# Optimization experiments

Hardware: AMD Instinct MI355X
Metric: run time of the kernel (lower is better)

## Reference

```python
import jax, jax.numpy as jnp
import numpy as np

# ---- static config ----
B, H, W, C = 32, 64, 64, 256
WS, SHIFT, NH = 8, 4, 8
HD = C // NH
N = WS * WS  # tokens per window
NW = (H // WS) * (W // WS)
EPS = 1e-5


def _relative_position_index(ws):
    ch, cw = np.meshgrid(np.arange(ws), np.arange(ws), indexing='ij')
    coords = np.stack([ch, cw]).reshape(2, -1)          # (2, N)
    rel = coords[:, :, None] - coords[:, None, :]        # (2, N, N)
    rel = rel.transpose(1, 2, 0)
    rel[:, :, 0] += ws - 1
    rel[:, :, 1] += ws - 1
    rel[:, :, 0] *= 2 * ws - 1
    return jnp.asarray(rel.sum(-1))                      # (N, N) int


def _shifted_window_mask(h, w, ws, shift):
    img = np.zeros((h, w))
    slices = (slice(0, -ws), slice(-ws, -shift), slice(-shift, None))
    cnt = 0
    for hs in slices:
        for wsl in slices:
            img[hs, wsl] = cnt
            cnt += 1
    mw = img.reshape(h // ws, ws, w // ws, ws).transpose(0, 2, 1, 3).reshape(-1, ws * ws)
    diff = mw[:, None, :] - mw[:, :, None]
    return jnp.asarray(np.where(diff != 0, -100.0, 0.0).astype(np.float32))  # (nW, N, N)


REL_IDX = _relative_position_index(WS)
ATTN_MASK = _shifted_window_mask(H, W, WS, SHIFT)


def _layernorm(x, g, b):
    mu = jnp.mean(x, axis=-1, keepdims=True)
    var = jnp.mean(jnp.square(x - mu), axis=-1, keepdims=True)
    return (x - mu) * jax.lax.rsqrt(var + EPS) * g + b


def _window_partition(x):  # (B,H,W,C) -> (B*nW, N, C)
    x = x.reshape(B, H // WS, WS, W // WS, WS, C)
    return x.transpose(0, 1, 3, 2, 4, 5).reshape(-1, N, C)


def _window_reverse(win):  # (B*nW, N, C) -> (B,H,W,C)
    x = win.reshape(B, H // WS, W // WS, WS, WS, C)
    return x.transpose(0, 1, 3, 2, 4, 5).reshape(B, H, W, C)


def setup_inputs() -> dict:
    key = jax.random.key(0)
    ks = jax.random.split(key, 6)
    s = lambda fan_in: 1.0 / np.sqrt(fan_in)
    return {
        'x': jax.random.normal(ks[0], (B, H * W, C), jnp.float32),
        'norm1_g': jnp.ones((C,), jnp.float32),
        'norm1_b': jnp.zeros((C,), jnp.float32),
        'qkv_w': jax.random.normal(ks[1], (C, 3 * C), jnp.float32) * s(C),
        'qkv_b': jnp.zeros((3 * C,), jnp.float32),
        'proj_w': jax.random.normal(ks[2], (C, C), jnp.float32) * s(C),
        'proj_b': jnp.zeros((C,), jnp.float32),
        'bias_table': jax.random.normal(ks[3], ((2 * WS - 1) ** 2, NH), jnp.float32) * 0.02,
        'norm2_g': jnp.ones((C,), jnp.float32),
        'norm2_b': jnp.zeros((C,), jnp.float32),
        'fc1_w': jax.random.normal(ks[4], (C, 4 * C), jnp.float32) * s(C),
        'fc1_b': jnp.zeros((4 * C,), jnp.float32),
        'fc2_w': jax.random.normal(ks[5], (4 * C, C), jnp.float32) * s(4 * C),
        'fc2_b': jnp.zeros((C,), jnp.float32),
    }


def reference(x, norm1_g, norm1_b, qkv_w, qkv_b, proj_w, proj_b, bias_table,
              norm2_g, norm2_b, fc1_w, fc1_b, fc2_w, fc2_b):
    shortcut = x
    h = _layernorm(x, norm1_g, norm1_b).reshape(B, H, W, C)
    # cyclic shift
    h = jnp.roll(h, shift=(-SHIFT, -SHIFT), axis=(1, 2))
    xw = _window_partition(h)                               # (Bw, N, C), Bw = B*nW
    # window attention
    qkv = xw @ qkv_w + qkv_b                                 # (Bw, N, 3C)
    qkv = qkv.reshape(-1, N, 3, NH, HD).transpose(2, 0, 3, 1, 4)
    q, k, v = qkv[0], qkv[1], qkv[2]                         # (Bw, NH, N, HD)
    attn = jnp.einsum('whnd,whmd->whnm', q * (HD ** -0.5), k)
    rpb = bias_table[REL_IDX.reshape(-1)].reshape(N, N, NH).transpose(2, 0, 1)
    attn = attn + rpb[None]
    attn = attn.reshape(B, NW, NH, N, N) + ATTN_MASK[None, :, None]
    attn = jax.nn.softmax(attn.reshape(-1, NH, N, N), axis=-1)
    out = jnp.einsum('whnm,whmd->whnd', attn, v)
    out = out.transpose(0, 2, 1, 3).reshape(-1, N, C)
    out = out @ proj_w + proj_b
    # reverse windows + shift back
    h = _window_reverse(out)
    h = jnp.roll(h, shift=(SHIFT, SHIFT), axis=(1, 2)).reshape(B, H * W, C)
    x = shortcut + h
    # MLP with pre-norm residual
    m = _layernorm(x, norm2_g, norm2_b)
    m = jax.nn.gelu(m @ fc1_w + fc1_b, approximate=False) @ fc2_w + fc2_b
    return x + m
```

## Files before the change

kernel.cpp:

```cpp
#include <hip/hip_runtime.h>
#include <hip/hip_bf16.h>


typedef __bf16 bf16;
typedef __bf16 bf16x8 __attribute__((ext_vector_type(8)));
typedef __bf16 bf16x4 __attribute__((ext_vector_type(4)));
typedef float  f32x4  __attribute__((ext_vector_type(4)));

#define GLDS(gp, lp)                                                                   \
    __builtin_amdgcn_global_load_lds(                                                  \
        (const __attribute__((address_space(1))) unsigned int*)(gp),                   \
        (__attribute__((address_space(3))) unsigned int*)(lp), 16, 0, 0)

__global__ __launch_bounds__(256) void prep_all(const float* __restrict__ qkv_w,
                                                const float* __restrict__ proj_w,
                                                const float* __restrict__ fc1_w,
                                                const float* __restrict__ fc2_w,
                                                const float* __restrict__ bt,
                                                bf16* __restrict__ WQ, bf16* __restrict__ WP,
                                                bf16* __restrict__ W1, bf16* __restrict__ W2,
                                                float* __restrict__ rpb) {
    int idx = blockIdx.x * 256 + threadIdx.x;
    if (idx < 196608) {
        int k = idx / 768, n = idx - k * 768;
        WQ[(size_t)n * 256 + k] = (bf16)qkv_w[idx];
    } else if (idx < 262144) {
        int l = idx - 196608;
        int k = l >> 8, n = l & 255;
        WP[(size_t)n * 256 + k] = (bf16)proj_w[l];
    } else if (idx < 524288) {
        int l = idx - 262144;
        int k = l >> 10, n = l & 1023;
        W1[(size_t)n * 256 + k] = (bf16)fc1_w[l];
    } else if (idx < 786432) {
        int l = idx - 524288;
        int k = l >> 8, n = l & 255;
        W2[(size_t)n * 1024 + k] = (bf16)fc2_w[l];
    } else {
        int l = idx - 786432;
        int h = l >> 12, n = (l >> 6) & 63, m = l & 63;
        int ridx = ((n >> 3) - (m >> 3) + 7) * 15 + ((n & 7) - (m & 7) + 7);
        rpb[l] = bt[ridx * 8 + h];
    }
}

__global__ __launch_bounds__(256) void ln_k(const float* __restrict__ x,
                                            const float* __restrict__ g,
                                            const float* __restrict__ bb,
                                            bf16* __restrict__ dst) {
    int t = blockIdx.x * 4 + (threadIdx.x >> 6);
    int lane = threadIdx.x & 63;
    int w = t >> 6, n = t & 63;
    int b = w >> 6, nw = w & 63;
    int r = ((nw >> 3) * 8 + (n >> 3) + 4) & 63;
    int c = ((nw & 7) * 8 + (n & 7) + 4) & 63;
    size_t src = ((size_t)b * 4096 + r * 64 + c) * 256;
    float4 v = *(const float4*)&x[src + lane * 4];
    float s = v.x + v.y + v.z + v.w;
    float sq = v.x * v.x + v.y * v.y + v.z * v.z + v.w * v.w;
#pragma unroll
    for (int off = 1; off < 64; off <<= 1) {
        s += __shfl_xor(s, off);
        sq += __shfl_xor(sq, off);
    }
    float mean = s * (1.0f / 256.0f);
    float var = sq * (1.0f / 256.0f) - mean * mean;
    float rstd = rsqrtf(var + 1e-5f);
    float4 gg = *(const float4*)&g[lane * 4];
    float4 bv = *(const float4*)&bb[lane * 4];
    bf16x4 o;
    o[0] = (bf16)((v.x - mean) * rstd * gg.x + bv.x);
    o[1] = (bf16)((v.y - mean) * rstd * gg.y + bv.y);
    o[2] = (bf16)((v.z - mean) * rstd * gg.z + bv.z);
    o[3] = (bf16)((v.w - mean) * rstd * gg.w + bv.w);
    *(bf16x4*)&dst[(size_t)t * 256 + lane * 4] = o;
}

__device__ __forceinline__ float fast_gelu(float v) {
    float t = v * v;
    float w = __builtin_fmaf(0.044715f * t, v, v);
    float e = __expf(-1.5957691216057308f * w);
    return v * __builtin_amdgcn_rcpf(1.0f + e);
}

template <int NDIM, int KDIM, int EPI>
__global__ __launch_bounds__(256) void gemm_k(const bf16* __restrict__ A,
                                              const bf16* __restrict__ Bt,
                                              const float* __restrict__ bias,
                                              bf16* __restrict__ outb,
                                              float* __restrict__ outf,
                                              const bf16* __restrict__ baseb) {
    __shared__ __align__(16) bf16 SH[24576];
    constexpr int NBN = NDIM / 128;
    constexpr int NK = KDIM / 32;
    const int tid = threadIdx.x;
    const int nwg = gridDim.x;
    const int flat = blockIdx.x;
    const int cpx = nwg >> 3;
    const int orig = (flat & 7) * cpx + (flat >> 3);
    const int bm = orig / NBN, bn = orig % NBN;

    const int lane = tid & 63, wid = tid >> 6;
    const int wr = wid >> 1, wc = wid & 1;
    const int lhi = lane >> 4, llo = lane & 15;

    f32x4 acc[4][4];
#pragma unroll
    for (int i = 0; i < 4; i++)
#pragma unroll
        for (int j = 0; j < 4; j++) acc[i][j] = f32x4{0.f, 0.f, 0.f, 0.f};

    const int srow = wid * 32 + (lane >> 2);
    const int scol = (((lane & 3) - ((lane >> 3) & 3)) & 3) * 8;
    const bf16* Ap = A + (size_t)(bm * 128 + srow) * KDIM + scol;
    const bf16* Bp = Bt + (size_t)(bn * 128 + srow) * KDIM + scol;
    const int gsw = ((lhi + (llo >> 1)) & 3) * 8;

#define STAGE(bufidx)                                                                  \
    do {                                                                               \
        bf16* Al = SH + (bufidx)*4096 + wid * 1024;                                    \
        bf16* Bl = SH + 12288 + (bufidx)*4096 + wid * 1024;                            \
        GLDS(Ap, Al);                                                                  \
        GLDS(Ap + 16 * KDIM, Al + 16 * 32);                                            \
        GLDS(Bp, Bl);                                                                  \
        GLDS(Bp + 16 * KDIM, Bl + 16 * 32);                                            \
        Ap += 32;                                                                      \
        Bp += 32;                                                                      \
    } while (0)

#define COMPUTE(bufidx)                                                                \
    do {                                                                               \
        const int ab = (bufidx)*4096;                                                  \
        bf16x8 af[4], bfr[4];                                                          \
        _Pragma("unroll") for (int mi = 0; mi < 4; mi++) af[mi] =                      \
            *(const bf16x8*)&SH[ab + (wr * 64 + mi * 16 + llo) * 32 + gsw];            \
        _Pragma("unroll") for (int ni = 0; ni < 4; ni++) bfr[ni] =                     \
            *(const bf16x8*)&SH[12288 + ab + (wc * 64 + ni * 16 + llo) * 32 + gsw];    \
        _Pragma("unroll") for (int mi = 0; mi < 4; mi++)                               \
            _Pragma("unroll") for (int ni = 0; ni < 4; ni++) acc[mi][ni] =             \
                __builtin_amdgcn_mfma_f32_16x16x32_bf16(bfr[ni], af[mi],               \
                                                        acc[mi][ni], 0, 0, 0);         \
    } while (0)

    STAGE(0);
    STAGE(1);
    int buf = 0;
    for (int i = 0; i < NK - 1; ++i) {
        asm volatile("s_waitcnt vmcnt(4) lgkmcnt(0)" ::: "memory");
        __builtin_amdgcn_s_barrier();
        __builtin_amdgcn_sched_barrier(0);
        if (i + 2 < NK) {
            const int sb = (buf + 2 >= 3) ? buf - 1 : buf + 2;
            STAGE(sb);
        }
        COMPUTE(buf);
        buf = (buf == 2) ? 0 : buf + 1;
    }
    asm volatile("s_waitcnt vmcnt(0) lgkmcnt(0)" ::: "memory");
    __builtin_amdgcn_s_barrier();
    __builtin_amdgcn_sched_barrier(0);
    COMPUTE(buf);

#undef STAGE
#undef COMPUTE

    __syncthreads();

    char* shb = (char*)SH;
    if constexpr (EPI == 0 || EPI == 2) {
#pragma unroll
        for (int ni = 0; ni < 4; ni++) {
            const int lcol = wc * 64 + ni * 16 + lhi * 4;
            const float4 b4 = *(const float4*)&bias[bn * 128 + lcol];
#pragma unroll
            for (int mi = 0; mi < 4; mi++) {
                const int ltok = wr * 64 + mi * 16 + llo;
                float v0 = acc[mi][ni][0] + b4.x;
                float v1 = acc[mi][ni][1] + b4.y;
                float v2 = acc[mi][ni][2] + b4.z;
                float v3 = acc[mi][ni][3] + b4.w;
                bf16x4 o;
                if constexpr (EPI == 2) {
                    o[0] = (bf16)fast_gelu(v0); o[1] = (bf16)fast_gelu(v1);
                    o[2] = (bf16)fast_gelu(v2); o[3] = (bf16)fast_gelu(v3);
                } else {
                    o[0] = (bf16)v0; o[1] = (bf16)v1; o[2] = (bf16)v2; o[3] = (bf16)v3;
                }
                const int u2 = (lcol >> 3) ^ (ltok & 15);
                *(bf16x4*)(shb + ltok * 256 + u2 * 16 + (lcol & 7) * 2) = o;
            }
        }
        __syncthreads();
        const int j = lane & 15;
#pragma unroll
        for (int rnd = 0; rnd < 8; rnd++) {
            const int ltok = wid * 32 + rnd * 4 + (lane >> 4);
            const int u2 = j ^ (ltok & 15);
            bf16x8 v = *(const bf16x8*)(shb + ltok * 256 + u2 * 16);
            *(bf16x8*)&outb[(size_t)(bm * 128 + ltok) * NDIM + bn * 128 + j * 8] = v;
        }
    } else {
#pragma unroll
        for (int p = 0; p < 2; p++) {
            if (wc == p) {
#pragma unroll
                for (int ni = 0; ni < 4; ni++) {
                    const int lcolh = ni * 16 + lhi * 4;
                    const float4 b4 = *(const float4*)&bias[bn * 128 + p * 64 + lcolh];
#pragma unroll
                    for (int mi = 0; mi < 4; mi++) {
                        const int ltok = wr * 64 + mi * 16 + llo;
                        float4 o = {acc[mi][ni][0] + b4.x, acc[mi][ni][1] + b4.y,
                                    acc[mi][ni][2] + b4.z, acc[mi][ni][3] + b4.w};
                        const int u2 = (lcolh >> 2) ^ (ltok & 15);
                        *(float4*)(shb + ltok * 256 + u2 * 16) = o;
                    }
                }
            }
            __syncthreads();
            const int j = lane & 15;
#pragma unroll
            for (int rnd = 0; rnd < 8; rnd++) {
                const int ltok = wid * 32 + rnd * 4 + (lane >> 4);
                const int u2 = j ^ (ltok & 15);
                float4 v = *(const float4*)(shb + ltok * 256 + u2 * 16);
                const int gcol = bn * 128 + p * 64 + j * 4;
                const int grow = bm * 128 + ltok;
                size_t dst = (size_t)grow * NDIM + gcol;
                bf16x4 bb = *(const bf16x4*)&baseb[dst];
                float4 o = {v.x + (float)bb[0], v.y + (float)bb[1],
                            v.z + (float)bb[2], v.w + (float)bb[3]};
                *(float4*)&outf[dst] = o;
            }
            if (p == 0) __syncthreads();
        }
    }
}

__global__ __launch_bounds__(256) void proj_ln_k(const bf16* __restrict__ A,
                                                 const bf16* __restrict__ Bt,
                                                 const float* __restrict__ bias,
                                                 const float* __restrict__ resid,
                                                 bf16* __restrict__ baseb,
                                                 const float* __restrict__ g2,
                                                 const float* __restrict__ b2,
                                                 bf16* __restrict__ hb) {
    __shared__ __align__(16) bf16 SH[32768];
    constexpr int KDIM = 256;
    const int tid = threadIdx.x;
    const int nwg = gridDim.x;
    const int flat = blockIdx.x;
    const int cpx = nwg >> 3;
    const int bm = (flat & 7) * cpx + (flat >> 3);

    const int lane = tid & 63, wid = tid >> 6;
    const int lhi = lane >> 4, llo = lane & 15;

    f32x4 acc[4][4];
#pragma unroll
    for (int i = 0; i < 4; i++)
#pragma unroll
        for (int j = 0; j < 4; j++) acc[i][j] = f32x4{0.f, 0.f, 0.f, 0.f};

    const int scol = (((lane & 3) - ((lane >> 3) & 3)) & 3) * 8;
    const bf16* Ap = A + (size_t)(bm * 64 + wid * 16 + (lane >> 2)) * KDIM + scol;
    const bf16* Bp = Bt + (size_t)(wid * 64 + (lane >> 2)) * KDIM + scol;
    const int gsw = ((lhi + (llo >> 1)) & 3) * 8;

#define PSTAGE(bufidx)                                                                 \
    do {                                                                               \
        bf16* Al = SH + (bufidx)*2048 + wid * 512;                                     \
        bf16* Bl = SH + 6144 + (bufidx)*8192 + wid * 2048;                             \
        GLDS(Ap, Al);                                                                  \
        GLDS(Bp, Bl);                                                                  \
        GLDS(Bp + 16 * KDIM, Bl + 512);                                                \
        GLDS(Bp + 32 * KDIM, Bl + 1024);                                               \
        GLDS(Bp + 48 * KDIM, Bl + 1536);                                               \
        Ap += 32;                                                                      \
        Bp += 32;                                                                      \
    } while (0)

#define PCOMPUTE(bufidx)                                                               \
    do {                                                                               \
        bf16x8 af[4], bfr[4];                                                          \
        _Pragma("unroll") for (int mi = 0; mi < 4; mi++) af[mi] =                      \
            *(const bf16x8*)&SH[(bufidx)*2048 + (mi * 16 + llo) * 32 + gsw];           \
        _Pragma("unroll") for (int ni = 0; ni < 4; ni++) bfr[ni] =                     \
            *(const bf16x8*)&SH[6144 + (bufidx)*8192 +                                 \
                                (wid * 64 + ni * 16 + llo) * 32 + gsw];                \
        _Pragma("unroll") for (int mi = 0; mi < 4; mi++)                               \
            _Pragma("unroll") for (int ni = 0; ni < 4; ni++) acc[mi][ni] =             \
                __builtin_amdgcn_mfma_f32_16x16x32_bf16(bfr[ni], af[mi],               \
                                                        acc[mi][ni], 0, 0, 0);         \
    } while (0)

#define PWAITBAR(N)                                                                    \
    asm volatile("s_waitcnt vmcnt(" #N ")" ::: "memory");                              \
    __builtin_amdgcn_s_barrier();                                                      \
    __builtin_amdgcn_sched_barrier(0)

    PSTAGE(0);
    PSTAGE(1);
    PSTAGE(2);
    int buf = 0;
    for (int i = 0; i + 3 < 8; ++i) {
        PWAITBAR(10);
        PCOMPUTE(buf);
        asm volatile("s_waitcnt lgkmcnt(0)" ::: "memory");
        __builtin_amdgcn_s_barrier();
        __builtin_amdgcn_sched_barrier(0);
        PSTAGE(buf);
        buf = (buf == 2) ? 0 : buf + 1;
    }
    PWAITBAR(10);
    PCOMPUTE(buf);
    buf = (buf == 2) ? 0 : buf + 1;
    PWAITBAR(5);
    PCOMPUTE(buf);
    buf = (buf == 2) ? 0 : buf + 1;
    PWAITBAR(0);
    PCOMPUTE(buf);

#undef PSTAGE
#undef PCOMPUTE
#undef PWAITBAR

    __syncthreads();

    char* shb = (char*)SH;
#pragma unroll
    for (int ni = 0; ni < 4; ni++) {
        const int col0 = wid * 64 + ni * 16 + lhi * 4;
        const float4 b4 = *(const float4*)&bias[col0];
#pragma unroll
        for (int mi = 0; mi < 4; mi++) {
            const int ltok = mi * 16 + llo;
            float4 o = {acc[mi][ni][0] + b4.x, acc[mi][ni][1] + b4.y,
                        acc[mi][ni][2] + b4.z, acc[mi][ni][3] + b4.w};
            const int u2 = (col0 >> 2) ^ (ltok & 15);
            *(float4*)(shb + ltok * 1024 + u2 * 16) = o;
        }
    }
    __syncthreads();

    const float4 gg = *(const float4*)&g2[lane * 4];
    const float4 bb4 = *(const float4*)&b2[lane * 4];
#pragma unroll
    for (int rnd = 0; rnd < 16; rnd++) {
        const int t = rnd * 4 + wid;
        const int u2 = lane ^ (t & 15);
        float4 v = *(const float4*)(shb + t * 1024 + u2 * 16);
        const int grow = bm * 64 + t;
        int w = grow >> 6, n = grow & 63;
        int b = w >> 6, nw = w & 63;
        int rr = ((nw >> 3) * 8 + (n >> 3) + 4) & 63;
        int cc = ((nw & 7) * 8 + (n & 7) + 4) & 63;
        const size_t rowbase = ((size_t)b * 4096 + rr * 64 + cc) * 256;
        float4 rs = *(const float4*)&resid[rowbase + lane * 4];
        float4 o = {rs.x + v.x, rs.y + v.y, rs.z + v.z, rs.w + v.w};
        bf16x4 bo = {(bf16)o.x, (bf16)o.y, (bf16)o.z, (bf16)o.w};
        *(bf16x4*)&baseb[rowbase + lane * 4] = bo;
        float s = o.x + o.y + o.z + o.w;
        float sq = o.x * o.x + o.y * o.y + o.z * o.z + o.w * o.w;
#pragma unroll
        for (int off = 1; off < 64; off <<= 1) {
            s += __shfl_xor(s, off);
            sq += __shfl_xor(sq, off);
        }
        float mean = s * (1.0f / 256.0f);
        float var = sq * (1.0f / 256.0f) - mean * mean;
        float rstd = rsqrtf(var + 1e-5f);
        bf16x4 ho;
        ho[0] = (bf16)((o.x - mean) * rstd * gg.x + bb4.x);
        ho[1] = (bf16)((o.y - mean) * rstd * gg.y + bb4.y);
        ho[2] = (bf16)((o.z - mean) * rstd * gg.z + bb4.z);
        ho[3] = (bf16)((o.w - mean) * rstd * gg.w + bb4.w);
        *(bf16x4*)&hb[rowbase + lane * 4] = ho;
    }
}

__device__ __forceinline__ int regid3(int p) { return p < 56 ? 0 : (p < 60 ? 1 : 2); }

__global__ __launch_bounds__(256) void attn_k(const bf16* __restrict__ qkv,
                                              const float* __restrict__ rpb,
                                              bf16* __restrict__ aout) {
    __shared__ __align__(16) bf16 Pl[4][64 * 80];
    const int wid = threadIdx.x >> 6, lane = threadIdx.x & 63;
    const int lhi = lane >> 4, llo = lane & 15;
    const int wh = blockIdx.x * 4 + wid;
    const int w = wh >> 3, h = wh & 7;
    const bf16* base = qkv + (size_t)w * (64 * 768);

    bf16x8 qf[4], kf[4];
#pragma unroll
    for (int i = 0; i < 4; i++)
        qf[i] = *(const bf16x8*)(base + (i * 16 + llo) * 768 + h * 32 + lhi * 8);
#pragma unroll
    for (int i = 0; i < 4; i++)
        kf[i] = *(const bf16x8*)(base + (i * 16 + llo) * 768 + 256 + h * 32 + lhi * 8);
    f32x4 s[4][4];
#pragma unroll
    for (int mi = 0; mi < 4; mi++)
#pragma unroll
        for (int ni = 0; ni < 4; ni++) {
            s[mi][ni] = f32x4{0.f, 0.f, 0.f, 0.f};
            s[mi][ni] =
                __builtin_amdgcn_mfma_f32_16x16x32_bf16(qf[mi], kf[ni], s[mi][ni], 0, 0, 0);
        }

    const int nw = w & 63;
    const int pr0 = (nw >> 3) * 8, pc0 = (nw & 7) * 8;
    int creg[4];
#pragma unroll
    for (int ni = 0; ni < 4; ni++) {
        int m = ni * 16 + llo;
        creg[ni] = regid3(pr0 + (m >> 3)) * 3 + regid3(pc0 + (m & 7));
    }
    float rmax[4][4], rsum[4][4];
#pragma unroll
    for (int mi = 0; mi < 4; mi++)
#pragma unroll
        for (int r = 0; r < 4; r++) {
            int n = mi * 16 + lhi * 4 + r;
            int rreg = regid3(pr0 + (n >> 3)) * 3 + regid3(pc0 + (n & 7));
            float mx = -1e30f;
#pragma unroll
            for (int ni = 0; ni < 4; ni++) {
                int m = ni * 16 + llo;
                float sv = s[mi][ni][r] * 0.17677669529663687f + rpb[(h * 64 + n) * 64 + m] +
                           (rreg == creg[ni] ? 0.0f : -100.0f);
                s[mi][ni][r] = sv;
                mx = fmaxf(mx, sv);
            }
            rmax[mi][r] = mx;
        }
#pragma unroll
    for (int off = 1; off < 16; off <<= 1)
#pragma unroll
        for (int mi = 0; mi < 4; mi++)
#pragma unroll
            for (int r = 0; r < 4; r++)
                rmax[mi][r] = fmaxf(rmax[mi][r], __shfl_xor(rmax[mi][r], off));
#pragma unroll
    for (int mi = 0; mi < 4; mi++)
#pragma unroll
        for (int r = 0; r < 4; r++) {
            float a = 0.f;
#pragma unroll
            for (int ni = 0; ni < 4; ni++) {
                float p = __expf(s[mi][ni][r] - rmax[mi][r]);
                s[mi][ni][r] = p;
                a += p;
            }
            rsum[mi][r] = a;
        }
#pragma unroll
    for (int off = 1; off < 16; off <<= 1)
#pragma unroll
        for (int mi = 0; mi < 4; mi++)
#pragma unroll
            for (int r = 0; r < 4; r++) rsum[mi][r] += __shfl_xor(rsum[mi][r], off);

    bf16* P = Pl[wid];
#pragma unroll
    for (int mi = 0; mi < 4; mi++)
#pragma unroll
        for (int r = 0; r < 4; r++) {
            float rinv = 1.0f / rsum[mi][r];
            int row = mi * 16 + lhi * 4 + r;
#pragma unroll
            for (int ni = 0; ni < 4; ni++)
                P[row * 80 + ni * 16 + llo] = (bf16)(s[mi][ni][r] * rinv);
        }

    f32x4 o[4][2];
#pragma unroll
    for (int mi = 0; mi < 4; mi++)
#pragma unroll
        for (int ni = 0; ni < 2; ni++) o[mi][ni] = f32x4{0.f, 0.f, 0.f, 0.f};
#pragma unroll
    for (int kc = 0; kc < 2; kc++) {
        bf16x8 pf[4], vf[2];
#pragma unroll
        for (int mi = 0; mi < 4; mi++)
            pf[mi] = *(const bf16x8*)(P + (mi * 16 + llo) * 80 + kc * 32 + lhi * 8);
#pragma unroll
        for (int ni = 0; ni < 2; ni++)
#pragma unroll
            for (int j = 0; j < 8; j++)
                vf[ni][j] = base[(kc * 32 + lhi * 8 + j) * 768 + 512 + h * 32 + ni * 16 + llo];
#pragma unroll
        for (int mi = 0; mi < 4; mi++)
#pragma unroll
            for (int ni = 0; ni < 2; ni++)
                o[mi][ni] =
                    __builtin_amdgcn_mfma_f32_16x16x32_bf16(pf[mi], vf[ni], o[mi][ni], 0, 0, 0);
    }
#pragma unroll
    for (int mi = 0; mi < 4; mi++)
#pragma unroll
        for (int ni = 0; ni < 2; ni++)
#pragma unroll
            for (int r = 0; r < 4; r++) {
                int row = mi * 16 + lhi * 4 + r;
                aout[(size_t)(w * 64 + row) * 256 + h * 32 + ni * 16 + llo] =
                    (bf16)o[mi][ni][r];
            }
}

extern "C" void kernel_launch(void* const* d_in, const int* in_sizes, int n_in,
                              void* d_out, int out_size, void* d_ws, size_t ws_size,
                              hipStream_t stream) {
    const float* x      = (const float*)d_in[0];
    const float* n1g    = (const float*)d_in[1];
    const float* n1b    = (const float*)d_in[2];
    const float* qkv_w  = (const float*)d_in[3];
    const float* qkv_b  = (const float*)d_in[4];
    const float* proj_w = (const float*)d_in[5];
    const float* proj_b = (const float*)d_in[6];
    const float* btab   = (const float*)d_in[7];
    const float* n2g    = (const float*)d_in[8];
    const float* n2b    = (const float*)d_in[9];
    const float* fc1_w  = (const float*)d_in[10];
    const float* fc1_b  = (const float*)d_in[11];
    const float* fc2_w  = (const float*)d_in[12];
    const float* fc2_b  = (const float*)d_in[13];
    float* out = (float*)d_out;
    char* ws = (char*)d_ws;

    constexpr size_t MB = 1048576ull;
    bf16* XWc   = (bf16*)(ws);
    bf16* QKVc  = (bf16*)(ws + 17 * MB);
    bf16* ATTNc = (bf16*)(ws + 68 * MB);
    bf16* BASEc = (bf16*)(ws + 85 * MB);
    bf16* Hbc   = (bf16*)(ws + 102 * MB);
    bf16* Gc    = (bf16*)(ws + 119 * MB);
    bf16* WQ    = (bf16*)(ws + 187 * MB);
    bf16* WP    = (bf16*)(ws + 187 * MB + 393216);
    bf16* W1    = (bf16*)(ws + 187 * MB + 524288);
    bf16* W2    = (bf16*)(ws + 187 * MB + 1048576);
    float* RPB  = (float*)(ws + 187 * MB + 1572864);

    dim3 blk(256);
    prep_all<<<3200, blk, 0, stream>>>(qkv_w, proj_w, fc1_w, fc2_w, btab,
                                       WQ, WP, W1, W2, RPB);

    for (int c = 0; c < 4; ++c) {
        const size_t xo = (size_t)c * 32768 * 256;
        ln_k<<<8192, blk, 0, stream>>>(x + xo, n1g, n1b, XWc);
        gemm_k<768, 256, 0><<<1536, blk, 0, stream>>>(XWc, WQ, qkv_b, QKVc,
                                                      nullptr, nullptr);
        attn_k<<<1024, blk, 0, stream>>>(QKVc, RPB, ATTNc);
        proj_ln_k<<<512, blk, 0, stream>>>(ATTNc, WP, proj_b, x + xo, BASEc,
                                           n2g, n2b, Hbc);
        gemm_k<1024, 256, 2><<<2048, blk, 0, stream>>>(Hbc, W1, fc1_b, Gc,
                                                       nullptr, nullptr);
        gemm_k<256, 1024, 3><<<512, blk, 0, stream>>>(Gc, W2, fc2_b, nullptr,
                                                      out + xo, BASEc);
    }
}
```

Before: 534.5 us.

## Widen GEMM tiles to 128x256 per workgroup with wider per-wave accumulators

The generic GEMM kernel now computes a 128x256 output tile instead of 128x128, with each wave holding 4x8 MFMA accumulators. This halves the grid sizes and reuses each A tile across twice as many columns. Shared memory grows to hold a double-width B tile, and the epilogues are rewritten for 256-wide rows with new swizzles. The cost is more registers and LDS per block, which lowers occupancy, plus fewer blocks per launch (256 for the fc2 GEMM), which may underfill the GPU.

```diff
diff --git a/kernel.cpp b/kernel.cpp
--- a/kernel.cpp
+++ b/kernel.cpp
@@ -84,14 +84,14 @@
 }
 
 template <int NDIM, int KDIM, int EPI>
-__global__ __launch_bounds__(256) void gemm_k(const bf16* __restrict__ A,
-                                              const bf16* __restrict__ Bt,
-                                              const float* __restrict__ bias,
-                                              bf16* __restrict__ outb,
-                                              float* __restrict__ outf,
-                                              const bf16* __restrict__ baseb) {
-    __shared__ __align__(16) bf16 SH[24576];
-    constexpr int NBN = NDIM / 128;
+__global__ __launch_bounds__(256, 2) void gemm_k(const bf16* __restrict__ A,
+                                                 const bf16* __restrict__ Bt,
+                                                 const float* __restrict__ bias,
+                                                 bf16* __restrict__ outb,
+                                                 float* __restrict__ outf,
+                                                 const bf16* __restrict__ baseb) {
+    __shared__ __align__(16) bf16 SH[36864];
+    constexpr int NBN = NDIM / 256;
     constexpr int NK = KDIM / 32;
     const int tid = threadIdx.x;
     const int nwg = gridDim.x;
@@ -104,40 +104,44 @@
     const int wr = wid >> 1, wc = wid & 1;
     const int lhi = lane >> 4, llo = lane & 15;
 
-    f32x4 acc[4][4];
+    f32x4 acc[4][8];
 #pragma unroll
     for (int i = 0; i < 4; i++)
 #pragma unroll
-        for (int j = 0; j < 4; j++) acc[i][j] = f32x4{0.f, 0.f, 0.f, 0.f};
+        for (int j = 0; j < 8; j++) acc[i][j] = f32x4{0.f, 0.f, 0.f, 0.f};
 
     const int srow = wid * 32 + (lane >> 2);
     const int scol = (((lane & 3) - ((lane >> 3) & 3)) & 3) * 8;
     const bf16* Ap = A + (size_t)(bm * 128 + srow) * KDIM + scol;
-    const bf16* Bp = Bt + (size_t)(bn * 128 + srow) * KDIM + scol;
+    const bf16* Bp0 = Bt + (size_t)(bn * 256 + srow) * KDIM + scol;
+    const bf16* Bp1 = Bt + (size_t)(bn * 256 + 128 + srow) * KDIM + scol;
     const int gsw = ((lhi + (llo >> 1)) & 3) * 8;
 
+    int koff = 0;
 #define STAGE(bufidx)                                                                  \
     do {                                                                               \
         bf16* Al = SH + (bufidx)*4096 + wid * 1024;                                    \
-        bf16* Bl = SH + 12288 + (bufidx)*4096 + wid * 1024;                            \
-        GLDS(Ap, Al);                                                                  \
-        GLDS(Ap + 16 * KDIM, Al + 16 * 32);                                            \
-        GLDS(Bp, Bl);                                                                  \
-        GLDS(Bp + 16 * KDIM, Bl + 16 * 32);                                            \
-        Ap += 32;                                                                      \
-        Bp += 32;                                                                      \
+        bf16* Bl = SH + 12288 + (bufidx)*8192 + wid * 1024;                            \
+        GLDS(Ap + koff, Al);                                                           \
+        GLDS(Ap + koff + 16 * KDIM, Al + 16 * 32);                                     \
+        GLDS(Bp0 + koff, Bl);                                                          \
+        GLDS(Bp0 + koff + 16 * KDIM, Bl + 16 * 32);                                    \
+        GLDS(Bp1 + koff, Bl + 4096);                                                   \
+        GLDS(Bp1 + koff + 16 * KDIM, Bl + 4096 + 16 * 32);                             \
+        koff += 32;                                                                    \
     } while (0)
 
 #define COMPUTE(bufidx)                                                                \
     do {                                                                               \
         const int ab = (bufidx)*4096;                                                  \
-        bf16x8 af[4], bfr[4];                                                          \
+        const int bb = 12288 + (bufidx)*8192;                                          \
+        bf16x8 af[4], bfr[8];                                                          \
         _Pragma("unroll") for (int mi = 0; mi < 4; mi++) af[mi] =                      \
             *(const bf16x8*)&SH[ab + (wr * 64 + mi * 16 + llo) * 32 + gsw];            \
-        _Pragma("unroll") for (int ni = 0; ni < 4; ni++) bfr[ni] =                     \
-            *(const bf16x8*)&SH[12288 + ab + (wc * 64 + ni * 16 + llo) * 32 + gsw];    \
+        _Pragma("unroll") for (int ni = 0; ni < 8; ni++) bfr[ni] =                     \
+            *(const bf16x8*)&SH[bb + (wc * 128 + ni * 16 + llo) * 32 + gsw];           \
         _Pragma("unroll") for (int mi = 0; mi < 4; mi++)                               \
-            _Pragma("unroll") for (int ni = 0; ni < 4; ni++) acc[mi][ni] =             \
+            _Pragma("unroll") for (int ni = 0; ni < 8; ni++) acc[mi][ni] =             \
                 __builtin_amdgcn_mfma_f32_16x16x32_bf16(bfr[ni], af[mi],               \
                                                         acc[mi][ni], 0, 0, 0);         \
     } while (0)
@@ -146,7 +150,7 @@
     STAGE(1);
     int buf = 0;
     for (int i = 0; i < NK - 1; ++i) {
-        asm volatile("s_waitcnt vmcnt(4) lgkmcnt(0)" ::: "memory");
+        asm volatile("s_waitcnt vmcnt(6) lgkmcnt(0)" ::: "memory");
         __builtin_amdgcn_s_barrier();
         __builtin_amdgcn_sched_barrier(0);
         if (i + 2 < NK) {
@@ -169,9 +173,9 @@
     char* shb = (char*)SH;
     if constexpr (EPI == 0 || EPI == 2) {
 #pragma unroll
-        for (int ni = 0; ni < 4; ni++) {
-            const int lcol = wc * 64 + ni * 16 + lhi * 4;
-            const float4 b4 = *(const float4*)&bias[bn * 128 + lcol];
+        for (int ni = 0; ni < 8; ni++) {
+            const int lcol = wc * 128 + ni * 16 + lhi * 4;
+            const float4 b4 = *(const float4*)&bias[bn * 256 + lcol];
 #pragma unroll
             for (int mi = 0; mi < 4; mi++) {
                 const int ltok = wr * 64 + mi * 16 + llo;
@@ -186,53 +190,50 @@
                 } else {
                     o[0] = (bf16)v0; o[1] = (bf16)v1; o[2] = (bf16)v2; o[3] = (bf16)v3;
                 }
-                const int u2 = (lcol >> 3) ^ (ltok & 15);
-                *(bf16x4*)(shb + ltok * 256 + u2 * 16 + (lcol & 7) * 2) = o;
+                const int u2 = (lcol >> 3) ^ (ltok & 31);
+                *(bf16x4*)(shb + ltok * 512 + u2 * 16 + (lcol & 7) * 2) = o;
             }
         }
         __syncthreads();
-        const int j = lane & 15;
-#pragma unroll
-        for (int rnd = 0; rnd < 8; rnd++) {
-            const int ltok = wid * 32 + rnd * 4 + (lane >> 4);
-            const int u2 = j ^ (ltok & 15);
-            bf16x8 v = *(const bf16x8*)(shb + ltok * 256 + u2 * 16);
-            *(bf16x8*)&outb[(size_t)(bm * 128 + ltok) * NDIM + bn * 128 + j * 8] = v;
+#pragma unroll
+        for (int it = 0; it < 16; it++) {
+            const int row = it * 8 + (tid >> 5);
+            const int g = tid & 31;
+            bf16x8 v = *(const bf16x8*)(shb + row * 512 + ((g ^ (row & 31)) << 4));
+            *(bf16x8*)&outb[(size_t)(bm * 128 + row) * NDIM + bn * 256 + g * 8] = v;
         }
     } else {
 #pragma unroll
         for (int p = 0; p < 2; p++) {
-            if (wc == p) {
-#pragma unroll
-                for (int ni = 0; ni < 4; ni++) {
-                    const int lcolh = ni * 16 + lhi * 4;
-                    const float4 b4 = *(const float4*)&bias[bn * 128 + p * 64 + lcolh];
+            if (p) __syncthreads();
+            if (wr == p) {
+#pragma unroll
+                for (int ni = 0; ni < 8; ni++) {
+                    const int g0 = wc * 32 + ni * 4 + lhi;
 #pragma unroll
                     for (int mi = 0; mi < 4; mi++) {
-                        const int ltok = wr * 64 + mi * 16 + llo;
-                        float4 o = {acc[mi][ni][0] + b4.x, acc[mi][ni][1] + b4.y,
-                                    acc[mi][ni][2] + b4.z, acc[mi][ni][3] + b4.w};
-                        const int u2 = (lcolh >> 2) ^ (ltok & 15);
-                        *(float4*)(shb + ltok * 256 + u2 * 16) = o;
+                        const int lrow = mi * 16 + llo;
+                        float4 o = {acc[mi][ni][0], acc[mi][ni][1], acc[mi][ni][2],
+                                    acc[mi][ni][3]};
+                        *(float4*)(shb + lrow * 1024 + ((g0 ^ (lrow & 31)) << 4)) = o;
                     }
                 }
             }
             __syncthreads();
-            const int j = lane & 15;
-#pragma unroll
-            for (int rnd = 0; rnd < 8; rnd++) {
-                const int ltok = wid * 32 + rnd * 4 + (lane >> 4);
-                const int u2 = j ^ (ltok & 15);
-                float4 v = *(const float4*)(shb + ltok * 256 + u2 * 16);
-                const int gcol = bn * 128 + p * 64 + j * 4;
-                const int grow = bm * 128 + ltok;
-                size_t dst = (size_t)grow * NDIM + gcol;
+#pragma unroll
+            for (int it = 0; it < 16; it++) {
+                const int lrow = it * 4 + (tid >> 6);
+                const int g = tid & 63;
+                float4 v = *(const float4*)(shb + lrow * 1024 + ((g ^ (lrow & 31)) << 4));
+                const int gcol = bn * 256 + g * 4;
+                const int grow = bm * 128 + p * 64 + lrow;
+                const float4 b4 = *(const float4*)&bias[gcol];
+                const size_t dst = (size_t)grow * NDIM + gcol;
                 bf16x4 bb = *(const bf16x4*)&baseb[dst];
-                float4 o = {v.x + (float)bb[0], v.y + (float)bb[1],
-                            v.z + (float)bb[2], v.w + (float)bb[3]};
+                float4 o = {v.x + b4.x + (float)bb[0], v.y + b4.y + (float)bb[1],
+                            v.z + b4.z + (float)bb[2], v.w + b4.w + (float)bb[3]};
                 *(float4*)&outf[dst] = o;
             }
-            if (p == 0) __syncthreads();
         }
     }
 }
@@ -548,14 +549,14 @@
     for (int c = 0; c < 4; ++c) {
         const size_t xo = (size_t)c * 32768 * 256;
         ln_k<<<8192, blk, 0, stream>>>(x + xo, n1g, n1b, XWc);
-        gemm_k<768, 256, 0><<<1536, blk, 0, stream>>>(XWc, WQ, qkv_b, QKVc,
-                                                      nullptr, nullptr);
+        gemm_k<768, 256, 0><<<768, blk, 0, stream>>>(XWc, WQ, qkv_b, QKVc,
+                                                     nullptr, nullptr);
         attn_k<<<1024, blk, 0, stream>>>(QKVc, RPB, ATTNc);
         proj_ln_k<<<512, blk, 0, stream>>>(ATTNc, WP, proj_b, x + xo, BASEc,
                                            n2g, n2b, Hbc);
-        gemm_k<1024, 256, 2><<<2048, blk, 0, stream>>>(Hbc, W1, fc1_b, Gc,
+        gemm_k<1024, 256, 2><<<1024, blk, 0, stream>>>(Hbc, W1, fc1_b, Gc,
                                                        nullptr, nullptr);
-        gemm_k<256, 1024, 3><<<512, blk, 0, stream>>>(Gc, W2, fc2_b, nullptr,
+        gemm_k<256, 1024, 3><<<256, blk, 0, stream>>>(Gc, W2, fc2_b, nullptr,
                                                       out + xo, BASEc);
     }
 }
```

Result: slower. 590.0 us (+10.4%).

## Fuse MLP fc1+GELU+fc2 into one kernel keeping hidden activations in LDS

Applied to the files above, without the earlier changes.

Replaces the separate fc1 (with GELU) and fc2 GEMM launches with a single mlp_k kernel. Each block takes 64 tokens, computes the 1024-wide hidden layer in chunks of 128 columns, applies GELU into LDS and accumulates fc2 directly. This removes the global round-trip of the large GELU intermediate. In exchange, fc2 weights are read straight from global memory without LDS staging, each block does more serial work, and there are only 512 blocks per chunk.

```diff
diff --git a/kernel.cpp b/kernel.cpp
--- a/kernel.cpp
+++ b/kernel.cpp
@@ -83,13 +83,11 @@
     return v * __builtin_amdgcn_rcpf(1.0f + e);
 }
 
-template <int NDIM, int KDIM, int EPI>
+template <int NDIM, int KDIM>
 __global__ __launch_bounds__(256) void gemm_k(const bf16* __restrict__ A,
                                               const bf16* __restrict__ Bt,
                                               const float* __restrict__ bias,
-                                              bf16* __restrict__ outb,
-                                              float* __restrict__ outf,
-                                              const bf16* __restrict__ baseb) {
+                                              bf16* __restrict__ outb) {
     __shared__ __align__(16) bf16 SH[24576];
     constexpr int NBN = NDIM / 128;
     constexpr int NK = KDIM / 32;
@@ -165,75 +163,179 @@
 #undef COMPUTE
 
     __syncthreads();
-
     char* shb = (char*)SH;
-    if constexpr (EPI == 0 || EPI == 2) {
-#pragma unroll
-        for (int ni = 0; ni < 4; ni++) {
-            const int lcol = wc * 64 + ni * 16 + lhi * 4;
-            const float4 b4 = *(const float4*)&bias[bn * 128 + lcol];
+#pragma unroll
+    for (int ni = 0; ni < 4; ni++) {
+        const int lcol = wc * 64 + ni * 16 + lhi * 4;
+        const float4 b4 = *(const float4*)&bias[bn * 128 + lcol];
+#pragma unroll
+        for (int mi = 0; mi < 4; mi++) {
+            const int ltok = wr * 64 + mi * 16 + llo;
+            bf16x4 o = {(bf16)(acc[mi][ni][0] + b4.x), (bf16)(acc[mi][ni][1] + b4.y),
+                        (bf16)(acc[mi][ni][2] + b4.z), (bf16)(acc[mi][ni][3] + b4.w)};
+            const int u2 = (lcol >> 3) ^ (ltok & 15);
+            *(bf16x4*)(shb + ltok * 256 + u2 * 16 + (lcol & 7) * 2) = o;
+        }
+    }
+    __syncthreads();
+    const int j = lane & 15;
+#pragma unroll
+    for (int rnd = 0; rnd < 8; rnd++) {
+        const int ltok = wid * 32 + rnd * 4 + (lane >> 4);
+        const int u2 = j ^ (ltok & 15);
+        bf16x8 v = *(const bf16x8*)(shb + ltok * 256 + u2 * 16);
+        *(bf16x8*)&outb[(size_t)(bm * 128 + ltok) * NDIM + bn * 128 + j * 8] = v;
+    }
+}
+
+__global__ __launch_bounds__(256, 2) void mlp_k(const bf16* __restrict__ Hs,
+                                                const bf16* __restrict__ W1t,
+                                                const float* __restrict__ b1,
+                                                const bf16* __restrict__ W2t,
+                                                const float* __restrict__ b2,
+                                                const bf16* __restrict__ baseb,
+                                                float* __restrict__ outf) {
+    __shared__ __align__(16) bf16 SH[32768];
+    const int tid = threadIdx.x;
+    const int nwg = gridDim.x;
+    const int flat = blockIdx.x;
+    const int cpx = nwg >> 3;
+    const int bm = (flat & 7) * cpx + (flat >> 3);
+
+    const int lane = tid & 63, wid = tid >> 6;
+    const int lhi = lane >> 4, llo = lane & 15;
+
+    const bf16* Hg = Hs + (size_t)bm * 64 * 256;
+#pragma unroll
+    for (int i = 0; i < 8; i++) {
+        const int f = i * 256 + tid;
+        const int row = f >> 5, phys = f & 31;
+        const int g = phys ^ (row & 31);
+        GLDS(Hg + row * 256 + g * 8, SH + f * 8);
+    }
+
+    f32x4 acc2[4][4];
+#pragma unroll
+    for (int i = 0; i < 4; i++)
+#pragma unroll
+        for (int j = 0; j < 4; j++) acc2[i][j] = f32x4{0.f, 0.f, 0.f, 0.f};
+
+    const int srow = wid * 32 + (lane >> 2);
+    const int scol = (((lane & 3) - ((lane >> 3) & 3)) & 3) * 8;
+    const int gsw = ((lhi + (llo >> 1)) & 3) * 8;
+
+    for (int c = 0; c < 8; ++c) {
+        const bf16* B1p = W1t + (size_t)(c * 128 + srow) * 256 + scol;
+        {
+            bf16* Bl = SH + 16384 + wid * 1024;
+            GLDS(B1p, Bl);
+            GLDS(B1p + 16 * 256, Bl + 16 * 32);
+        }
+        f32x4 gacc[4][2];
+#pragma unroll
+        for (int i = 0; i < 4; i++) {
+            gacc[i][0] = f32x4{0.f, 0.f, 0.f, 0.f};
+            gacc[i][1] = f32x4{0.f, 0.f, 0.f, 0.f};
+        }
+
+        for (int ks = 0; ks < 8; ++ks) {
+            asm volatile("s_waitcnt vmcnt(0) lgkmcnt(0)" ::: "memory");
+            __builtin_amdgcn_s_barrier();
+            __builtin_amdgcn_sched_barrier(0);
+            const int buf = ks & 1;
+            if (ks + 1 < 8) {
+                bf16* Bl = SH + 16384 + (buf ^ 1) * 4096 + wid * 1024;
+                GLDS(B1p + (ks + 1) * 32, Bl);
+                GLDS(B1p + (ks + 1) * 32 + 16 * 256, Bl + 16 * 32);
+            }
+            bf16x8 af[4], bfr[2];
 #pragma unroll
             for (int mi = 0; mi < 4; mi++) {
-                const int ltok = wr * 64 + mi * 16 + llo;
-                float v0 = acc[mi][ni][0] + b4.x;
-                float v1 = acc[mi][ni][1] + b4.y;
-                float v2 = acc[mi][ni][2] + b4.z;
-                float v3 = acc[mi][ni][3] + b4.w;
+                const int row = mi * 16 + llo;
+                const int phys = (ks * 4 + lhi) ^ (row & 31);
+                af[mi] = *(const bf16x8*)&SH[row * 256 + phys * 8];
+            }
+#pragma unroll
+            for (int ni = 0; ni < 2; ni++)
+                bfr[ni] = *(const bf16x8*)&SH[16384 + buf * 4096 +
+                                              (wid * 32 + ni * 16 + llo) * 32 + gsw];
+#pragma unroll
+            for (int mi = 0; mi < 4; mi++)
+#pragma unroll
+                for (int ni = 0; ni < 2; ni++)
+                    gacc[mi][ni] = __builtin_amdgcn_mfma_f32_16x16x32_bf16(
+                        bfr[ni], af[mi], gacc[mi][ni], 0, 0, 0);
+        }
+
+        char* Gb = (char*)(SH + 24576);
+#pragma unroll
+        for (int ni = 0; ni < 2; ni++) {
+            const int col0 = wid * 32 + ni * 16 + lhi * 4;
+            const float4 b4 = *(const float4*)&b1[c * 128 + col0];
+#pragma unroll
+            for (int mi = 0; mi < 4; mi++) {
+                const int token = mi * 16 + llo;
                 bf16x4 o;
-                if constexpr (EPI == 2) {
-                    o[0] = (bf16)fast_gelu(v0); o[1] = (bf16)fast_gelu(v1);
-                    o[2] = (bf16)fast_gelu(v2); o[3] = (bf16)fast_gelu(v3);
-                } else {
-                    o[0] = (bf16)v0; o[1] = (bf16)v1; o[2] = (bf16)v2; o[3] = (bf16)v3;
-                }
-                const int u2 = (lcol >> 3) ^ (ltok & 15);
-                *(bf16x4*)(shb + ltok * 256 + u2 * 16 + (lcol & 7) * 2) = o;
+                o[0] = (bf16)fast_gelu(gacc[mi][ni][0] + b4.x);
+                o[1] = (bf16)fast_gelu(gacc[mi][ni][1] + b4.y);
+                o[2] = (bf16)fast_gelu(gacc[mi][ni][2] + b4.z);
+                o[3] = (bf16)fast_gelu(gacc[mi][ni][3] + b4.w);
+                const int phys = (col0 >> 3) ^ (token & 15);
+                *(bf16x4*)(Gb + token * 256 + phys * 16 + (col0 & 7) * 2) = o;
             }
         }
         __syncthreads();
-        const int j = lane & 15;
-#pragma unroll
-        for (int rnd = 0; rnd < 8; rnd++) {
-            const int ltok = wid * 32 + rnd * 4 + (lane >> 4);
-            const int u2 = j ^ (ltok & 15);
-            bf16x8 v = *(const bf16x8*)(shb + ltok * 256 + u2 * 16);
-            *(bf16x8*)&outb[(size_t)(bm * 128 + ltok) * NDIM + bn * 128 + j * 8] = v;
-        }
-    } else {
-#pragma unroll
-        for (int p = 0; p < 2; p++) {
-            if (wc == p) {
-#pragma unroll
-                for (int ni = 0; ni < 4; ni++) {
-                    const int lcolh = ni * 16 + lhi * 4;
-                    const float4 b4 = *(const float4*)&bias[bn * 128 + p * 64 + lcolh];
-#pragma unroll
-                    for (int mi = 0; mi < 4; mi++) {
-                        const int ltok = wr * 64 + mi * 16 + llo;
-                        float4 o = {acc[mi][ni][0] + b4.x, acc[mi][ni][1] + b4.y,
-                                    acc[mi][ni][2] + b4.z, acc[mi][ni][3] + b4.w};
-                        const int u2 = (lcolh >> 2) ^ (ltok & 15);
-                        *(float4*)(shb + ltok * 256 + u2 * 16) = o;
-                    }
-                }
+
+#pragma unroll
+        for (int ks2 = 0; ks2 < 4; ++ks2) {
+            bf16x8 af2[4], bfr2[4];
+#pragma unroll
+            for (int mi = 0; mi < 4; mi++) {
+                const int row = mi * 16 + llo;
+                const int phys = (ks2 * 4 + lhi) ^ (row & 15);
+                af2[mi] = *(const bf16x8*)&SH[24576 + row * 128 + phys * 8];
             }
-            __syncthreads();
-            const int j = lane & 15;
-#pragma unroll
-            for (int rnd = 0; rnd < 8; rnd++) {
-                const int ltok = wid * 32 + rnd * 4 + (lane >> 4);
-                const int u2 = j ^ (ltok & 15);
-                float4 v = *(const float4*)(shb + ltok * 256 + u2 * 16);
-                const int gcol = bn * 128 + p * 64 + j * 4;
-                const int grow = bm * 128 + ltok;
-                size_t dst = (size_t)grow * NDIM + gcol;
-                bf16x4 bb = *(const bf16x4*)&baseb[dst];
-                float4 o = {v.x + (float)bb[0], v.y + (float)bb[1],
-                            v.z + (float)bb[2], v.w + (float)bb[3]};
-                *(float4*)&outf[dst] = o;
-            }
-            if (p == 0) __syncthreads();
-        }
+#pragma unroll
+            for (int ni = 0; ni < 4; ni++)
+                bfr2[ni] = *(const bf16x8*)&W2t[(size_t)(wid * 64 + ni * 16 + llo) * 1024 +
+                                                c * 128 + ks2 * 32 + lhi * 8];
+#pragma unroll
+            for (int mi = 0; mi < 4; mi++)
+#pragma unroll
+                for (int ni = 0; ni < 4; ni++)
+                    acc2[mi][ni] = __builtin_amdgcn_mfma_f32_16x16x32_bf16(
+                        bfr2[ni], af2[mi], acc2[mi][ni], 0, 0, 0);
+        }
+        __syncthreads();
+    }
+
+    char* shb = (char*)SH;
+#pragma unroll
+    for (int ni = 0; ni < 4; ni++) {
+        const int g0 = wid * 16 + ni * 4 + lhi;
+#pragma unroll
+        for (int mi = 0; mi < 4; mi++) {
+            const int row = mi * 16 + llo;
+            const int phys = g0 ^ (row & 31);
+            float4 o = {acc2[mi][ni][0], acc2[mi][ni][1], acc2[mi][ni][2],
+                        acc2[mi][ni][3]};
+            *(float4*)(shb + row * 1024 + phys * 16) = o;
+        }
+    }
+    __syncthreads();
+#pragma unroll
+    for (int it = 0; it < 16; it++) {
+        const int f = it * 256 + tid;
+        const int row = f >> 6, g = f & 63;
+        const int phys = g ^ (row & 31);
+        float4 v = *(const float4*)(shb + row * 1024 + phys * 16);
+        const int gcol = g * 4;
+        const size_t dst = (size_t)(bm * 64 + row) * 256 + gcol;
+        const float4 b4 = *(const float4*)&b2[gcol];
+        bf16x4 bb = *(const bf16x4*)&baseb[dst];
+        float4 o = {v.x + b4.x + (float)bb[0], v.y + b4.y + (float)bb[1],
+                    v.z + b4.z + (float)bb[2], v.w + b4.w + (float)bb[3]};
+        *(float4*)&outf[dst] = o;
     }
 }
 
@@ -534,12 +636,11 @@
     bf16* ATTNc = (bf16*)(ws + 68 * MB);
     bf16* BASEc = (bf16*)(ws + 85 * MB);
     bf16* Hbc   = (bf16*)(ws + 102 * MB);
-    bf16* Gc    = (bf16*)(ws + 119 * MB);
-    bf16* WQ    = (bf16*)(ws + 187 * MB);
-    bf16* WP    = (bf16*)(ws + 187 * MB + 393216);
-    bf16* W1    = (bf16*)(ws + 187 * MB + 524288);
-    bf16* W2    = (bf16*)(ws + 187 * MB + 1048576);
-    float* RPB  = (float*)(ws + 187 * MB + 1572864);
+    bf16* WQ    = (bf16*)(ws + 119 * MB);
+    bf16* WP    = (bf16*)(ws + 119 * MB + 393216);
+    bf16* W1    = (bf16*)(ws + 119 * MB + 524288);
+    bf16* W2    = (bf16*)(ws + 119 * MB + 1048576);
+    float* RPB  = (float*)(ws + 119 * MB + 1572864);
 
     dim3 blk(256);
     prep_all<<<3200, blk, 0, stream>>>(qkv_w, proj_w, fc1_w, fc2_w, btab,
@@ -548,14 +649,10 @@
     for (int c = 0; c < 4; ++c) {
         const size_t xo = (size_t)c * 32768 * 256;
         ln_k<<<8192, blk, 0, stream>>>(x + xo, n1g, n1b, XWc);
-        gemm_k<768, 256, 0><<<1536, blk, 0, stream>>>(XWc, WQ, qkv_b, QKVc,
-                                                      nullptr, nullptr);
+        gemm_k<768, 256><<<1536, blk, 0, stream>>>(XWc, WQ, qkv_b, QKVc);
         attn_k<<<1024, blk, 0, stream>>>(QKVc, RPB, ATTNc);
         proj_ln_k<<<512, blk, 0, stream>>>(ATTNc, WP, proj_b, x + xo, BASEc,
                                            n2g, n2b, Hbc);
-        gemm_k<1024, 256, 2><<<2048, blk, 0, stream>>>(Hbc, W1, fc1_b, Gc,
-                                                       nullptr, nullptr);
-        gemm_k<256, 1024, 3><<<512, blk, 0, stream>>>(Gc, W2, fc2_b, nullptr,
-                                                      out + xo, BASEc);
-    }
-}
+        mlp_k<<<512, blk, 0, stream>>>(Hbc, W1, fc1_b, W2, fc2_b, BASEc, out + xo);
+    }
+}
```

Measured after the change: 566.8 us. 1.06x slower.
